# Performance work log

Hardware: AMD Instinct MI355X
Metric: run time of the kernel (lower is better)

Reference implementation:

```python
import jax, jax.numpy as jnp
import numpy as np

DIM = 128
NUM_HEADS = 8
HEAD_DIM = DIM // NUM_HEADS
N_NODES = 50000
N_EDGES = 800000


def setup_inputs() -> dict:
    key = jax.random.key(0)
    ks = jax.random.split(key, 10)
    scale = 1.0 / np.sqrt(DIM)
    x = jax.random.normal(ks[0], (N_NODES, DIM), dtype=jnp.float32)
    edge_index = jax.random.randint(ks[1], (2, N_EDGES), 0, N_NODES, dtype=jnp.int64)
    Wq = jax.random.normal(ks[2], (DIM, DIM), dtype=jnp.float32) * scale
    bq = jnp.zeros((DIM,), dtype=jnp.float32)
    Wk = jax.random.normal(ks[3], (DIM, DIM), dtype=jnp.float32) * scale
    bk = jnp.zeros((DIM,), dtype=jnp.float32)
    Wv = jax.random.normal(ks[4], (DIM, DIM), dtype=jnp.float32) * scale
    bv = jnp.zeros((DIM,), dtype=jnp.float32)
    Wo = jax.random.normal(ks[5], (DIM, DIM), dtype=jnp.float32) * scale
    bo = jnp.zeros((DIM,), dtype=jnp.float32)
    return {"x": x, "edge_index": edge_index, "Wq": Wq, "bq": bq,
            "Wk": Wk, "bk": bk, "Wv": Wv, "bv": bv, "Wo": Wo, "bo": bo}


def reference(x, edge_index, Wq, bq, Wk, bk, Wv, bv, Wo, bo):
    n = x.shape[0]
    tgt = edge_index[0]  # softmax group / scatter destination
    src = edge_index[1]  # gather source
    # projections: torch nn.Linear -> x @ W.T + b
    q = (x @ Wq.T + bq).reshape(n, NUM_HEADS, HEAD_DIM)
    k = (x @ Wk.T + bk).reshape(n, NUM_HEADS, HEAD_DIM)
    v = (x @ Wv.T + bv).reshape(n, NUM_HEADS, HEAD_DIM)
    # edge-wise attention scores: [E, H]
    scores = jnp.einsum('ehd,ehd->eh', q[src], k[tgt]) / np.sqrt(HEAD_DIM).astype(np.float32)
    # segment softmax over edges grouped by target node
    m = jax.ops.segment_max(scores, tgt, num_segments=n)          # [N, H]
    m = jax.lax.stop_gradient(m)
    p = jnp.exp(scores - m[tgt])                                   # [E, H]
    s = jax.ops.segment_sum(p, tgt, num_segments=n)               # [N, H]
    probs = p / s[tgt]
    # weighted scatter-add of source values
    weighted = v[src] * probs[..., None]                           # [E, H, D]
    agg = jax.ops.segment_sum(weighted, tgt, num_segments=n)      # [N, H, D]
    out = agg.reshape(n, DIM) @ Wo.T + bo
    # dropout is identity in eval mode
    return out
```

## Files before the change

kernel.cpp:

```cpp
#include <hip/hip_runtime.h>
#include <math.h>

#define NN 50000
#define NE 800000
#define DIM 128
#define NH 8
#define HD 16
#define NTILE 3125
#define TPB 782
#define LROW 136
#define QVROW 256
#define SCAN_B 196

typedef short v8s __attribute__((ext_vector_type(8)));
typedef float v4f __attribute__((ext_vector_type(4)));

__device__ __forceinline__ unsigned short f2b(float f) {
    unsigned u = __float_as_uint(f);
    u = (u + 0x7fffu + ((u >> 16) & 1u)) >> 16;
    return (unsigned short)u;
}
__device__ __forceinline__ float blo(unsigned w) { return __uint_as_float(w << 16); }
__device__ __forceinline__ float bhi(unsigned w) { return __uint_as_float(w & 0xffff0000u); }

template<int PAT>
__device__ __forceinline__ float swz(float x) {
    return __int_as_float(__builtin_amdgcn_ds_swizzle(__float_as_int(x), PAT));
}

#define NW4 (4 * DIM * DIM / 4)
#define NC4 ((NN + 3) / 4)
__global__ __launch_bounds__(256) void convert_kernel(
    const float* __restrict__ Wq, const float* __restrict__ Wk,
    const float* __restrict__ Wv, const float* __restrict__ Wo,
    unsigned short* __restrict__ Wb, int* __restrict__ cnt)
{
    int i = blockIdx.x * 256 + threadIdx.x;
    if (i < NW4) {
        int mat = i >> 12;
        int off = i & 4095;
        const float* Wsrc = (mat == 0) ? Wq : (mat == 1) ? Wk : (mat == 2) ? Wv : Wo;
        float4 f = ((const float4*)Wsrc)[off];
        uint2 o;
        o.x = (unsigned)f2b(f.x) | ((unsigned)f2b(f.y) << 16);
        o.y = (unsigned)f2b(f.z) | ((unsigned)f2b(f.w) << 16);
        ((uint2*)(Wb + (size_t)mat * DIM * DIM))[off] = o;
    } else if (i < NW4 + NC4) {
        ((int4*)cnt)[i - NW4] = make_int4(0, 0, 0, 0);
    }
}

__global__ __launch_bounds__(256) void qkv_mfma_kernel(
    const float* __restrict__ x, const unsigned short* __restrict__ Wb,
    const float* __restrict__ bq, const float* __restrict__ bk, const float* __restrict__ bv,
    unsigned short* __restrict__ qvb, unsigned short* __restrict__ kb,
    const int* __restrict__ tgt, int* __restrict__ cnt, int* __restrict__ rank)
{
    __shared__ unsigned short Wl[DIM * LROW];
    const int mat = blockIdx.x / TPB;
    const int tg  = blockIdx.x % TPB;
    const int tid = threadIdx.x;
    const int lane = tid & 63;
    const int warp = tid >> 6;
    const int m = lane & 15;
    const int quad = lane >> 4;

    const int gsize = 3 * TPB * 256;
    for (int e = blockIdx.x * 256 + tid; e < NE; e += gsize)
        rank[e] = atomicAdd(cnt + tgt[e], 1);

    const unsigned short* Wg = Wb + (size_t)mat * DIM * DIM;
#pragma unroll
    for (int it = 0; it < 8; ++it) {
        int chunk = it * 256 + tid;
        int row = chunk >> 4, c8 = chunk & 15;
        *(uint4*)(Wl + row * LROW + c8 * 8) = ((const uint4*)Wg)[chunk];
    }
    __syncthreads();

    const int rt = tg * 4 + warp;
    if (rt >= NTILE) return;
    const int r0 = rt * 16;

    const float* bias_p = (mat == 0) ? bq : (mat == 1) ? bk : bv;

    v8s a[4];
#pragma unroll
    for (int kt = 0; kt < 4; ++kt) {
        const float4* xr = (const float4*)(x + (size_t)(r0 + m) * DIM + kt * 32 + quad * 8);
        float4 f0 = xr[0], f1 = xr[1];
        v8s t;
        t[0] = (short)f2b(f0.x); t[1] = (short)f2b(f0.y);
        t[2] = (short)f2b(f0.z); t[3] = (short)f2b(f0.w);
        t[4] = (short)f2b(f1.x); t[5] = (short)f2b(f1.y);
        t[6] = (short)f2b(f1.z); t[7] = (short)f2b(f1.w);
        a[kt] = t;
    }

    const int i0 = (lane & 1) ? 2 : 0;

#pragma unroll
    for (int nt = 0; nt < 8; ++nt) {
        v4f c = {0.f, 0.f, 0.f, 0.f};
#pragma unroll
        for (int kt = 0; kt < 4; ++kt) {
            v8s b = *(const v8s*)(Wl + (nt * 16 + m) * LROW + kt * 32 + quad * 8);
            c = __builtin_amdgcn_mfma_f32_16x16x32_bf16(a[kt], b, c, 0, 0, 0);
        }
        int col = nt * 16 + m;
        float bias = bias_p[col];
        unsigned w0 = 0, w1 = 0;
#pragma unroll
        for (int i = 0; i < 4; ++i) {
            unsigned own  = (unsigned)f2b(c[i] + bias);
            unsigned part = (unsigned)__builtin_amdgcn_ds_swizzle((int)own, 0x041F) & 0xffffu;
            unsigned w = (lane & 1) ? (part | (own << 16)) : (own | (part << 16));
            if (i == i0)     w0 = w;
            if (i == i0 + 1) w1 = w;
        }
        int colb = nt * 16 + (m & ~1);
        int rowa = r0 + quad * 4 + i0;
        if (mat == 1) {
            *(unsigned*)(kb + (size_t)rowa * DIM + colb)       = w0;
            *(unsigned*)(kb + (size_t)(rowa + 1) * DIM + colb) = w1;
        } else {
            int pos = colb * 2 + ((mat == 2) ? 2 : 0);
            *(unsigned*)(qvb + (size_t)rowa * QVROW + pos)       = w0;
            *(unsigned*)(qvb + (size_t)(rowa + 1) * QVROW + pos) = w1;
        }
    }
}

__global__ __launch_bounds__(256) void scan1_kernel(
    const int* __restrict__ cnt, int* __restrict__ off, int* __restrict__ bsum)
{
    __shared__ int ws4[4];
    const int tid = threadIdx.x, lane = tid & 63, wid = tid >> 6;
    int i = blockIdx.x * 256 + tid;
    int v0 = (i < NN) ? cnt[i] : 0;
    int incl = v0;
#pragma unroll
    for (int d = 1; d < 64; d <<= 1) {
        int t = __shfl_up(incl, d);
        if (lane >= d) incl += t;
    }
    if (lane == 63) ws4[wid] = incl;
    __syncthreads();
    int wexcl = 0;
#pragma unroll
    for (int t = 0; t < 3; ++t) if (t < wid) wexcl += ws4[t];
    if (i < NN) off[i] = wexcl + incl - v0;
    if (tid == 255) bsum[blockIdx.x] = wexcl + incl;
}

__global__ __launch_bounds__(256) void scan23_kernel(
    const int* __restrict__ bsum, int* __restrict__ off)
{
    __shared__ int ws4[4];
    __shared__ int base_s, total_s;
    const int tid = threadIdx.x, lane = tid & 63, wid = tid >> 6;
    int v0 = (tid < SCAN_B) ? bsum[tid] : 0;
    int incl = v0;
#pragma unroll
    for (int d = 1; d < 64; d <<= 1) {
        int t = __shfl_up(incl, d);
        if (lane >= d) incl += t;
    }
    if (lane == 63) ws4[wid] = incl;
    __syncthreads();
    int wexcl = 0;
#pragma unroll
    for (int t = 0; t < 3; ++t) if (t < wid) wexcl += ws4[t];
    int excl = wexcl + incl - v0;
    if (tid == blockIdx.x) base_s = excl;
    if (tid == SCAN_B - 1) total_s = excl + v0;
    __syncthreads();
    int i = blockIdx.x * 256 + tid;
    if (i < NN) off[i] += base_s;
    if (blockIdx.x == SCAN_B - 1 && tid == 0) off[NN] = total_s;
}

__global__ __launch_bounds__(256) void fill_kernel(
    const int* __restrict__ tgt, const int* __restrict__ src,
    const int* __restrict__ off, const int* __restrict__ rank,
    int* __restrict__ edge_src)
{
    int e = blockIdx.x * 256 + threadIdx.x;
    if (e >= NE) return;
    int pos = off[tgt[e]] + rank[e];
    edge_src[pos] = src[e];
}

__global__ __launch_bounds__(256) void attn_kernel(
    const int* __restrict__ off, const int* __restrict__ edge_src,
    const unsigned short* __restrict__ qvb, const unsigned short* __restrict__ kb,
    unsigned short* __restrict__ aggb)
{
    const int tid = threadIdx.x;
    const int lane = tid & 63;
    const int node = blockIdx.x * 4 + (tid >> 6);
    if (node >= NN) return;

    const int base = __builtin_amdgcn_readfirstlane(off[node]);
    const int deg  = __builtin_amdgcn_readfirstlane(off[node + 1]) - base;

    unsigned kw = *(const unsigned*)(kb + (size_t)node * DIM + 2 * lane);
    const float klo = blo(kw), khi = bhi(kw);
    const int j = lane & 7;

    float ax = 0.f, ay = 0.f, ss = 0.f;

    uint2 qv[8];

#define G1(BB, I) { \
        int si = __builtin_amdgcn_readlane(srcv, (BB) * 8 + (I)); \
        qv[I] = ((const uint2*)(qvb + ((size_t)(unsigned)si << 8)))[lane]; }

#define ACC1(I) { float pi = swz<((I) << 5) | 0x18>(p); \
        unsigned vv = qv[I].y; ax += pi * blo(vv); ay += pi * bhi(vv); }

    for (int c0 = 0; c0 < deg; c0 += 64) {
        const int nchunk = min(deg - c0, 64);
        int srcv = edge_src[base + min(c0 + lane, deg - 1)];
        const int nbt = (nchunk + 7) >> 3;
        for (int bb = 0; bb < nbt; ++bb) {
            G1(bb, 0) G1(bb, 1) G1(bb, 2) G1(bb, 3)
            G1(bb, 4) G1(bb, 5) G1(bb, 6) G1(bb, 7)
            const int nbu = nchunk - bb * 8;
            float part0 = blo(qv[0].x) * klo + bhi(qv[0].x) * khi;
            float part1 = blo(qv[1].x) * klo + bhi(qv[1].x) * khi;
            float part2 = blo(qv[2].x) * klo + bhi(qv[2].x) * khi;
            float part3 = blo(qv[3].x) * klo + bhi(qv[3].x) * khi;
            float part4 = blo(qv[4].x) * klo + bhi(qv[4].x) * khi;
            float part5 = blo(qv[5].x) * klo + bhi(qv[5].x) * khi;
            float part6 = blo(qv[6].x) * klo + bhi(qv[6].x) * khi;
            float part7 = blo(qv[7].x) * klo + bhi(qv[7].x) * khi;
            float r10 = ((j & 1) ? part1 : part0) + swz<0x041F>((j & 1) ? part0 : part1);
            float r11 = ((j & 1) ? part3 : part2) + swz<0x041F>((j & 1) ? part2 : part3);
            float r12 = ((j & 1) ? part5 : part4) + swz<0x041F>((j & 1) ? part4 : part5);
            float r13 = ((j & 1) ? part7 : part6) + swz<0x041F>((j & 1) ? part6 : part7);
            float r20 = ((j & 2) ? r11 : r10) + swz<0x081F>((j & 2) ? r10 : r11);
            float r21 = ((j & 2) ? r13 : r12) + swz<0x081F>((j & 2) ? r12 : r13);
            float tot = ((j & 4) ? r21 : r20) + swz<0x101F>((j & 4) ? r20 : r21);
            float p = (j < nbu) ? __expf(tot * 0.25f) : 0.f;
            ss += p;
            ACC1(0) ACC1(1) ACC1(2) ACC1(3)
            ACC1(4) ACC1(5) ACC1(6) ACC1(7)
        }
    }
#undef G1
#undef ACC1

    ss += swz<0x041F>(ss);
    ss += swz<0x081F>(ss);
    ss += swz<0x101F>(ss);

    unsigned* ap = (unsigned*)(aggb + (size_t)node * DIM + 2 * lane);
    if (deg == 0) {
        *ap = 0u;
    } else {
        float inv = 1.f / ss;
        *ap = (unsigned)f2b(ax * inv) | ((unsigned)f2b(ay * inv) << 16);
    }
}

__global__ __launch_bounds__(256) void outproj_mfma_kernel(
    const unsigned short* __restrict__ aggb, const unsigned short* __restrict__ Wob,
    const float* __restrict__ bo, float* __restrict__ out)
{
    __shared__ unsigned short Wl[DIM * LROW];
    const int tid = threadIdx.x;
    const int lane = tid & 63;
    const int warp = tid >> 6;
    const int m = lane & 15;
    const int quad = lane >> 4;

#pragma unroll
    for (int it = 0; it < 8; ++it) {
        int chunk = it * 256 + tid;
        int row = chunk >> 4, c8 = chunk & 15;
        *(uint4*)(Wl + row * LROW + c8 * 8) = ((const uint4*)Wob)[chunk];
    }
    __syncthreads();

    const int rt = blockIdx.x * 4 + warp;
    if (rt >= NTILE) return;
    const int r0 = rt * 16;

    v8s a[4];
#pragma unroll
    for (int kt = 0; kt < 4; ++kt)
        a[kt] = *(const v8s*)(aggb + (size_t)(r0 + m) * DIM + kt * 32 + quad * 8);

#pragma unroll
    for (int nt = 0; nt < 8; ++nt) {
        v4f c = {0.f, 0.f, 0.f, 0.f};
#pragma unroll
        for (int kt = 0; kt < 4; ++kt) {
            v8s b = *(const v8s*)(Wl + (nt * 16 + m) * LROW + kt * 32 + quad * 8);
            c = __builtin_amdgcn_mfma_f32_16x16x32_bf16(a[kt], b, c, 0, 0, 0);
        }
        int col = nt * 16 + m;
        float bias = bo[col];
#pragma unroll
        for (int i = 0; i < 4; ++i) {
            int row = r0 + quad * 4 + i;
            out[(size_t)row * DIM + col] = c[i] + bias;
        }
    }
}

extern "C" void kernel_launch(void* const* d_in, const int* in_sizes, int n_in,
                              void* d_out, int out_size, void* d_ws, size_t ws_size,
                              hipStream_t stream) {
    const float* x  = (const float*)d_in[0];
    const int*   ei = (const int*)d_in[1];
    const float* Wq = (const float*)d_in[2];
    const float* bq = (const float*)d_in[3];
    const float* Wk = (const float*)d_in[4];
    const float* bk = (const float*)d_in[5];
    const float* Wv = (const float*)d_in[6];
    const float* bv = (const float*)d_in[7];
    const float* Wo = (const float*)d_in[8];
    const float* bo = (const float*)d_in[9];

    const int* tgt = ei;
    const int* src = ei + NE;

    char* ws = (char*)d_ws;
    const size_t SZ_QV = (size_t)NN * QVROW * 2;
    const size_t SZ_BF = (size_t)NN * DIM * 2;

    unsigned short* qvb  = (unsigned short*)(ws);
    unsigned short* kb   = (unsigned short*)(ws + SZ_QV);
    unsigned short* aggb = (unsigned short*)(ws + SZ_QV + SZ_BF);
    unsigned short* Wb   = (unsigned short*)(ws + SZ_QV + 2 * SZ_BF);

    char* wi = ws + SZ_QV + 2 * SZ_BF + (size_t)4 * DIM * DIM * 2;
    int* cnt      = (int*)(wi);
    int* off      = (int*)(wi + (size_t)NN * 4);
    int* rank     = (int*)(wi + (size_t)(2 * NN + 1) * 4);
    int* edge_src = (int*)(wi + (size_t)(2 * NN + 1 + NE) * 4);
    int* bsum     = (int*)(wi + (size_t)(2 * NN + 1 + 2 * NE) * 4);

    const int conv_blocks = (NW4 + NC4 + 255) / 256;
    const int edge_blocks = (NE + 255) / 256;

    convert_kernel<<<conv_blocks, 256, 0, stream>>>(Wq, Wk, Wv, Wo, Wb, cnt);
    qkv_mfma_kernel<<<3 * TPB, 256, 0, stream>>>(x, Wb, bq, bk, bv, qvb, kb, tgt, cnt, rank);
    scan1_kernel<<<SCAN_B, 256, 0, stream>>>(cnt, off, bsum);
    scan23_kernel<<<SCAN_B, 256, 0, stream>>>(bsum, off);
    fill_kernel<<<edge_blocks, 256, 0, stream>>>(tgt, src, off, rank, edge_src);
    attn_kernel<<<(NN + 3) / 4, 256, 0, stream>>>(off, edge_src, qvb, kb, aggb);
    outproj_mfma_kernel<<<TPB, 256, 0, stream>>>(
        aggb, Wb + (size_t)3 * DIM * DIM, bo, (float*)d_out);
}
```

Measured before the change: 218.9 us.

## Stage projection weights in two LDS halves to cut shared memory per block

The QKV and output projection kernels now hold only 64 rows of the bf16 weight matrix in LDS at a time and process the output columns in two passes, with a barrier between reloads. This halves LDS use per block (about 17KB instead of 34KB), so more blocks can be resident per CU. The x/agg loads are issued before the first weight load so they can overlap it. Inactive warps no longer return early, because they must still take part in the barriers. The cost is an extra barrier and a serialized second weight load per block.

```diff
diff --git a/kernel.cpp b/kernel.cpp
--- a/kernel.cpp
+++ b/kernel.cpp
@@ -56,7 +56,7 @@
     unsigned short* __restrict__ qvb, unsigned short* __restrict__ kb,
     const int* __restrict__ tgt, int* __restrict__ cnt, int* __restrict__ rank)
 {
-    __shared__ unsigned short Wl[DIM * LROW];
+    __shared__ unsigned short Wl[64 * LROW];
     const int mat = blockIdx.x / TPB;
     const int tg  = blockIdx.x % TPB;
     const int tid = threadIdx.x;
@@ -70,63 +70,72 @@
         rank[e] = atomicAdd(cnt + tgt[e], 1);
 
     const unsigned short* Wg = Wb + (size_t)mat * DIM * DIM;
-#pragma unroll
-    for (int it = 0; it < 8; ++it) {
-        int chunk = it * 256 + tid;
-        int row = chunk >> 4, c8 = chunk & 15;
-        *(uint4*)(Wl + row * LROW + c8 * 8) = ((const uint4*)Wg)[chunk];
-    }
-    __syncthreads();
-
     const int rt = tg * 4 + warp;
-    if (rt >= NTILE) return;
+    const bool act = (rt < NTILE);
     const int r0 = rt * 16;
 
     const float* bias_p = (mat == 0) ? bq : (mat == 1) ? bk : bv;
 
     v8s a[4];
-#pragma unroll
-    for (int kt = 0; kt < 4; ++kt) {
-        const float4* xr = (const float4*)(x + (size_t)(r0 + m) * DIM + kt * 32 + quad * 8);
-        float4 f0 = xr[0], f1 = xr[1];
-        v8s t;
-        t[0] = (short)f2b(f0.x); t[1] = (short)f2b(f0.y);
-        t[2] = (short)f2b(f0.z); t[3] = (short)f2b(f0.w);
-        t[4] = (short)f2b(f1.x); t[5] = (short)f2b(f1.y);
-        t[6] = (short)f2b(f1.z); t[7] = (short)f2b(f1.w);
-        a[kt] = t;
+    if (act) {
+#pragma unroll
+        for (int kt = 0; kt < 4; ++kt) {
+            const float4* xr = (const float4*)(x + (size_t)(r0 + m) * DIM + kt * 32 + quad * 8);
+            float4 f0 = xr[0], f1 = xr[1];
+            v8s t;
+            t[0] = (short)f2b(f0.x); t[1] = (short)f2b(f0.y);
+            t[2] = (short)f2b(f0.z); t[3] = (short)f2b(f0.w);
+            t[4] = (short)f2b(f1.x); t[5] = (short)f2b(f1.y);
+            t[6] = (short)f2b(f1.z); t[7] = (short)f2b(f1.w);
+            a[kt] = t;
+        }
     }
 
     const int i0 = (lane & 1) ? 2 : 0;
 
 #pragma unroll
-    for (int nt = 0; nt < 8; ++nt) {
-        v4f c = {0.f, 0.f, 0.f, 0.f};
-#pragma unroll
-        for (int kt = 0; kt < 4; ++kt) {
-            v8s b = *(const v8s*)(Wl + (nt * 16 + m) * LROW + kt * 32 + quad * 8);
-            c = __builtin_amdgcn_mfma_f32_16x16x32_bf16(a[kt], b, c, 0, 0, 0);
-        }
-        int col = nt * 16 + m;
-        float bias = bias_p[col];
-        unsigned w0 = 0, w1 = 0;
-#pragma unroll
-        for (int i = 0; i < 4; ++i) {
-            unsigned own  = (unsigned)f2b(c[i] + bias);
-            unsigned part = (unsigned)__builtin_amdgcn_ds_swizzle((int)own, 0x041F) & 0xffffu;
-            unsigned w = (lane & 1) ? (part | (own << 16)) : (own | (part << 16));
-            if (i == i0)     w0 = w;
-            if (i == i0 + 1) w1 = w;
-        }
-        int colb = nt * 16 + (m & ~1);
-        int rowa = r0 + quad * 4 + i0;
-        if (mat == 1) {
-            *(unsigned*)(kb + (size_t)rowa * DIM + colb)       = w0;
-            *(unsigned*)(kb + (size_t)(rowa + 1) * DIM + colb) = w1;
-        } else {
-            int pos = colb * 2 + ((mat == 2) ? 2 : 0);
-            *(unsigned*)(qvb + (size_t)rowa * QVROW + pos)       = w0;
-            *(unsigned*)(qvb + (size_t)(rowa + 1) * QVROW + pos) = w1;
+    for (int h = 0; h < 2; ++h) {
+        if (h) __syncthreads();
+#pragma unroll
+        for (int it = 0; it < 4; ++it) {
+            int chunk = h * 1024 + it * 256 + tid;
+            int row = (chunk >> 4) - h * 64, c8 = chunk & 15;
+            *(uint4*)(Wl + row * LROW + c8 * 8) = ((const uint4*)Wg)[chunk];
+        }
+        __syncthreads();
+
+        if (act) {
+#pragma unroll
+            for (int ntl = 0; ntl < 4; ++ntl) {
+                const int nt = h * 4 + ntl;
+                v4f c = {0.f, 0.f, 0.f, 0.f};
+#pragma unroll
+                for (int kt = 0; kt < 4; ++kt) {
+                    v8s b = *(const v8s*)(Wl + (ntl * 16 + m) * LROW + kt * 32 + quad * 8);
+                    c = __builtin_amdgcn_mfma_f32_16x16x32_bf16(a[kt], b, c, 0, 0, 0);
+                }
+                int col = nt * 16 + m;
+                float bias = bias_p[col];
+                unsigned w0 = 0, w1 = 0;
+#pragma unroll
+                for (int i = 0; i < 4; ++i) {
+                    unsigned own  = (unsigned)f2b(c[i] + bias);
+                    unsigned part = (unsigned)__builtin_amdgcn_ds_swizzle((int)own, 0x041F) & 0xffffu;
+                    unsigned w = (lane & 1) ? (part | (own << 16)) : (own | (part << 16));
+                    if (i == i0)     w0 = w;
+                    if (i == i0 + 1) w1 = w;
+                }
+                int colb = nt * 16 + (m & ~1);
+                int rowa = r0 + quad * 4 + i0;
+                if (mat == 1) {
+                    *(unsigned*)(kb + (size_t)rowa * DIM + colb)       = w0;
+                    *(unsigned*)(kb + (size_t)(rowa + 1) * DIM + colb) = w1;
+                } else {
+                    int pos = colb * 2 + ((mat == 2) ? 2 : 0);
+                    *(unsigned*)(qvb + (size_t)rowa * QVROW + pos)       = w0;
+                    *(unsigned*)(qvb + (size_t)(rowa + 1) * QVROW + pos) = w1;
+                }
+            }
         }
     }
 }
@@ -268,44 +277,53 @@
     const unsigned short* __restrict__ aggb, const unsigned short* __restrict__ Wob,
     const float* __restrict__ bo, float* __restrict__ out)
 {
-    __shared__ unsigned short Wl[DIM * LROW];
+    __shared__ unsigned short Wl[64 * LROW];
     const int tid = threadIdx.x;
     const int lane = tid & 63;
     const int warp = tid >> 6;
     const int m = lane & 15;
     const int quad = lane >> 4;
 
-#pragma unroll
-    for (int it = 0; it < 8; ++it) {
-        int chunk = it * 256 + tid;
-        int row = chunk >> 4, c8 = chunk & 15;
-        *(uint4*)(Wl + row * LROW + c8 * 8) = ((const uint4*)Wob)[chunk];
-    }
-    __syncthreads();
-
     const int rt = blockIdx.x * 4 + warp;
-    if (rt >= NTILE) return;
+    const bool act = (rt < NTILE);
     const int r0 = rt * 16;
 
     v8s a[4];
-#pragma unroll
-    for (int kt = 0; kt < 4; ++kt)
-        a[kt] = *(const v8s*)(aggb + (size_t)(r0 + m) * DIM + kt * 32 + quad * 8);
-
-#pragma unroll
-    for (int nt = 0; nt < 8; ++nt) {
-        v4f c = {0.f, 0.f, 0.f, 0.f};
-#pragma unroll
-        for (int kt = 0; kt < 4; ++kt) {
-            v8s b = *(const v8s*)(Wl + (nt * 16 + m) * LROW + kt * 32 + quad * 8);
-            c = __builtin_amdgcn_mfma_f32_16x16x32_bf16(a[kt], b, c, 0, 0, 0);
-        }
-        int col = nt * 16 + m;
-        float bias = bo[col];
-#pragma unroll
-        for (int i = 0; i < 4; ++i) {
-            int row = r0 + quad * 4 + i;
-            out[(size_t)row * DIM + col] = c[i] + bias;
+    if (act) {
+#pragma unroll
+        for (int kt = 0; kt < 4; ++kt)
+            a[kt] = *(const v8s*)(aggb + (size_t)(r0 + m) * DIM + kt * 32 + quad * 8);
+    }
+
+#pragma unroll
+    for (int h = 0; h < 2; ++h) {
+        if (h) __syncthreads();
+#pragma unroll
+        for (int it = 0; it < 4; ++it) {
+            int chunk = h * 1024 + it * 256 + tid;
+            int row = (chunk >> 4) - h * 64, c8 = chunk & 15;
+            *(uint4*)(Wl + row * LROW + c8 * 8) = ((const uint4*)Wob)[chunk];
+        }
+        __syncthreads();
+
+        if (act) {
+#pragma unroll
+            for (int ntl = 0; ntl < 4; ++ntl) {
+                const int nt = h * 4 + ntl;
+                v4f c = {0.f, 0.f, 0.f, 0.f};
+#pragma unroll
+                for (int kt = 0; kt < 4; ++kt) {
+                    v8s b = *(const v8s*)(Wl + (ntl * 16 + m) * LROW + kt * 32 + quad * 8);
+                    c = __builtin_amdgcn_mfma_f32_16x16x32_bf16(a[kt], b, c, 0, 0, 0);
+                }
+                int col = nt * 16 + m;
+                float bias = bo[col];
+#pragma unroll
+                for (int i = 0; i < 4; ++i) {
+                    int row = r0 + quad * 4 + i;
+                    out[(size_t)row * DIM + col] = c[i] + bias;
+                }
+            }
         }
     }
 }
```

New measurement: 219.6 us. About the same (+0.3%).

## Fuse edge attention aggregation with output projection via shared-memory tile

Applied to the files above, without the earlier changes.

Merges the attention kernel and the output-projection MFMA kernel. Each block processes 16 nodes, with each wave handling 4 nodes in sequence, and writes the aggregated bf16 rows into a shared-memory tile. The block then runs the MFMA out-projection with each wave computing 2 column tiles, reading Wo directly from global memory. This removes the global agg buffer round-trip and one kernel launch. The cost is less parallelism per wave, since each wave now walks 4 nodes serially, and a block barrier that can stall on high-degree nodes.

```diff
diff --git a/kernel.cpp b/kernel.cpp
--- a/kernel.cpp
+++ b/kernel.cpp
@@ -191,113 +191,98 @@
     edge_src[pos] = src[e];
 }
 
-__global__ __launch_bounds__(256) void attn_kernel(
+__global__ __launch_bounds__(256) void attn_out_kernel(
     const int* __restrict__ off, const int* __restrict__ edge_src,
     const unsigned short* __restrict__ qvb, const unsigned short* __restrict__ kb,
-    unsigned short* __restrict__ aggb)
-{
+    const unsigned short* __restrict__ Wob, const float* __restrict__ bo,
+    float* __restrict__ out)
+{
+    __shared__ unsigned short aggL[16 * LROW];
     const int tid = threadIdx.x;
     const int lane = tid & 63;
-    const int node = blockIdx.x * 4 + (tid >> 6);
-    if (node >= NN) return;
-
-    const int base = __builtin_amdgcn_readfirstlane(off[node]);
-    const int deg  = __builtin_amdgcn_readfirstlane(off[node + 1]) - base;
-
-    unsigned kw = *(const unsigned*)(kb + (size_t)node * DIM + 2 * lane);
-    const float klo = blo(kw), khi = bhi(kw);
+    const int w = tid >> 6;
+    const int r0 = blockIdx.x * 16;
     const int j = lane & 7;
-
-    float ax = 0.f, ay = 0.f, ss = 0.f;
 
     uint2 qv[8];
 
 #define G1(BB, I) { \
         int si = __builtin_amdgcn_readlane(srcv, (BB) * 8 + (I)); \
         qv[I] = ((const uint2*)(qvb + ((size_t)(unsigned)si << 8)))[lane]; }
-
 #define ACC1(I) { float pi = swz<((I) << 5) | 0x18>(p); \
         unsigned vv = qv[I].y; ax += pi * blo(vv); ay += pi * bhi(vv); }
 
-    for (int c0 = 0; c0 < deg; c0 += 64) {
-        const int nchunk = min(deg - c0, 64);
-        int srcv = edge_src[base + min(c0 + lane, deg - 1)];
-        const int nbt = (nchunk + 7) >> 3;
-        for (int bb = 0; bb < nbt; ++bb) {
-            G1(bb, 0) G1(bb, 1) G1(bb, 2) G1(bb, 3)
-            G1(bb, 4) G1(bb, 5) G1(bb, 6) G1(bb, 7)
-            const int nbu = nchunk - bb * 8;
-            float part0 = blo(qv[0].x) * klo + bhi(qv[0].x) * khi;
-            float part1 = blo(qv[1].x) * klo + bhi(qv[1].x) * khi;
-            float part2 = blo(qv[2].x) * klo + bhi(qv[2].x) * khi;
-            float part3 = blo(qv[3].x) * klo + bhi(qv[3].x) * khi;
-            float part4 = blo(qv[4].x) * klo + bhi(qv[4].x) * khi;
-            float part5 = blo(qv[5].x) * klo + bhi(qv[5].x) * khi;
-            float part6 = blo(qv[6].x) * klo + bhi(qv[6].x) * khi;
-            float part7 = blo(qv[7].x) * klo + bhi(qv[7].x) * khi;
-            float r10 = ((j & 1) ? part1 : part0) + swz<0x041F>((j & 1) ? part0 : part1);
-            float r11 = ((j & 1) ? part3 : part2) + swz<0x041F>((j & 1) ? part2 : part3);
-            float r12 = ((j & 1) ? part5 : part4) + swz<0x041F>((j & 1) ? part4 : part5);
-            float r13 = ((j & 1) ? part7 : part6) + swz<0x041F>((j & 1) ? part6 : part7);
-            float r20 = ((j & 2) ? r11 : r10) + swz<0x081F>((j & 2) ? r10 : r11);
-            float r21 = ((j & 2) ? r13 : r12) + swz<0x081F>((j & 2) ? r12 : r13);
-            float tot = ((j & 4) ? r21 : r20) + swz<0x101F>((j & 4) ? r20 : r21);
-            float p = (j < nbu) ? __expf(tot * 0.25f) : 0.f;
-            ss += p;
-            ACC1(0) ACC1(1) ACC1(2) ACC1(3)
-            ACC1(4) ACC1(5) ACC1(6) ACC1(7)
+#pragma unroll
+    for (int i = 0; i < 4; ++i) {
+        const int node = r0 + w * 4 + i;
+        const int base = __builtin_amdgcn_readfirstlane(off[node]);
+        const int deg  = __builtin_amdgcn_readfirstlane(off[node + 1]) - base;
+
+        unsigned kw = *(const unsigned*)(kb + (size_t)node * DIM + 2 * lane);
+        const float klo = blo(kw), khi = bhi(kw);
+        float ax = 0.f, ay = 0.f, ss = 0.f;
+
+        for (int c0 = 0; c0 < deg; c0 += 64) {
+            const int nchunk = min(deg - c0, 64);
+            int srcv = edge_src[base + min(c0 + lane, deg - 1)];
+            const int nbt = (nchunk + 7) >> 3;
+            for (int bb = 0; bb < nbt; ++bb) {
+                G1(bb, 0) G1(bb, 1) G1(bb, 2) G1(bb, 3)
+                G1(bb, 4) G1(bb, 5) G1(bb, 6) G1(bb, 7)
+                const int nbu = nchunk - bb * 8;
+                float part0 = blo(qv[0].x) * klo + bhi(qv[0].x) * khi;
+                float part1 = blo(qv[1].x) * klo + bhi(qv[1].x) * khi;
+                float part2 = blo(qv[2].x) * klo + bhi(qv[2].x) * khi;
+                float part3 = blo(qv[3].x) * klo + bhi(qv[3].x) * khi;
+                float part4 = blo(qv[4].x) * klo + bhi(qv[4].x) * khi;
+                float part5 = blo(qv[5].x) * klo + bhi(qv[5].x) * khi;
+                float part6 = blo(qv[6].x) * klo + bhi(qv[6].x) * khi;
+                float part7 = blo(qv[7].x) * klo + bhi(qv[7].x) * khi;
+                float r10 = ((j & 1) ? part1 : part0) + swz<0x041F>((j & 1) ? part0 : part1);
+                float r11 = ((j & 1) ? part3 : part2) + swz<0x041F>((j & 1) ? part2 : part3);
+                float r12 = ((j & 1) ? part5 : part4) + swz<0x041F>((j & 1) ? part4 : part5);
+                float r13 = ((j & 1) ? part7 : part6) + swz<0x041F>((j & 1) ? part6 : part7);
+                float r20 = ((j & 2) ? r11 : r10) + swz<0x081F>((j & 2) ? r10 : r11);
+                float r21 = ((j & 2) ? r13 : r12) + swz<0x081F>((j & 2) ? r12 : r13);
+                float tot = ((j & 4) ? r21 : r20) + swz<0x101F>((j & 4) ? r20 : r21);
+                float p = (j < nbu) ? __expf(tot * 0.25f) : 0.f;
+                ss += p;
+                ACC1(0) ACC1(1) ACC1(2) ACC1(3)
+                ACC1(4) ACC1(5) ACC1(6) ACC1(7)
+            }
+        }
+        ss += swz<0x041F>(ss);
+        ss += swz<0x081F>(ss);
+        ss += swz<0x101F>(ss);
+
+        unsigned* ap = (unsigned*)(aggL + (w * 4 + i) * LROW + 2 * lane);
+        if (deg == 0) {
+            *ap = 0u;
+        } else {
+            float inv = 1.f / ss;
+            *ap = (unsigned)f2b(ax * inv) | ((unsigned)f2b(ay * inv) << 16);
         }
     }
 #undef G1
 #undef ACC1
 
-    ss += swz<0x041F>(ss);
-    ss += swz<0x081F>(ss);
-    ss += swz<0x101F>(ss);
-
-    unsigned* ap = (unsigned*)(aggb + (size_t)node * DIM + 2 * lane);
-    if (deg == 0) {
-        *ap = 0u;
-    } else {
-        float inv = 1.f / ss;
-        *ap = (unsigned)f2b(ax * inv) | ((unsigned)f2b(ay * inv) << 16);
-    }
-}
-
-__global__ __launch_bounds__(256) void outproj_mfma_kernel(
-    const unsigned short* __restrict__ aggb, const unsigned short* __restrict__ Wob,
-    const float* __restrict__ bo, float* __restrict__ out)
-{
-    __shared__ unsigned short Wl[DIM * LROW];
-    const int tid = threadIdx.x;
-    const int lane = tid & 63;
-    const int warp = tid >> 6;
+    __syncthreads();
+
     const int m = lane & 15;
     const int quad = lane >> 4;
 
-#pragma unroll
-    for (int it = 0; it < 8; ++it) {
-        int chunk = it * 256 + tid;
-        int row = chunk >> 4, c8 = chunk & 15;
-        *(uint4*)(Wl + row * LROW + c8 * 8) = ((const uint4*)Wob)[chunk];
-    }
-    __syncthreads();
-
-    const int rt = blockIdx.x * 4 + warp;
-    if (rt >= NTILE) return;
-    const int r0 = rt * 16;
-
     v8s a[4];
 #pragma unroll
     for (int kt = 0; kt < 4; ++kt)
-        a[kt] = *(const v8s*)(aggb + (size_t)(r0 + m) * DIM + kt * 32 + quad * 8);
-
-#pragma unroll
-    for (int nt = 0; nt < 8; ++nt) {
+        a[kt] = *(const v8s*)(aggL + m * LROW + kt * 32 + quad * 8);
+
+#pragma unroll
+    for (int t = 0; t < 2; ++t) {
+        const int nt = w * 2 + t;
         v4f c = {0.f, 0.f, 0.f, 0.f};
 #pragma unroll
         for (int kt = 0; kt < 4; ++kt) {
-            v8s b = *(const v8s*)(Wl + (nt * 16 + m) * LROW + kt * 32 + quad * 8);
+            v8s b = *(const v8s*)(Wob + (size_t)(nt * 16 + m) * DIM + kt * 32 + quad * 8);
             c = __builtin_amdgcn_mfma_f32_16x16x32_bf16(a[kt], b, c, 0, 0, 0);
         }
         int col = nt * 16 + m;
@@ -333,10 +318,9 @@
 
     unsigned short* qvb  = (unsigned short*)(ws);
     unsigned short* kb   = (unsigned short*)(ws + SZ_QV);
-    unsigned short* aggb = (unsigned short*)(ws + SZ_QV + SZ_BF);
-    unsigned short* Wb   = (unsigned short*)(ws + SZ_QV + 2 * SZ_BF);
-
-    char* wi = ws + SZ_QV + 2 * SZ_BF + (size_t)4 * DIM * DIM * 2;
+    unsigned short* Wb   = (unsigned short*)(ws + SZ_QV + SZ_BF);
+
+    char* wi = ws + SZ_QV + SZ_BF + (size_t)4 * DIM * DIM * 2;
     int* cnt      = (int*)(wi);
     int* off      = (int*)(wi + (size_t)NN * 4);
     int* rank     = (int*)(wi + (size_t)(2 * NN + 1) * 4);
@@ -351,7 +335,6 @@
     scan1_kernel<<<SCAN_B, 256, 0, stream>>>(cnt, off, bsum);
     scan23_kernel<<<SCAN_B, 256, 0, stream>>>(bsum, off);
     fill_kernel<<<edge_blocks, 256, 0, stream>>>(tgt, src, off, rank, edge_src);
-    attn_kernel<<<(NN + 3) / 4, 256, 0, stream>>>(off, edge_src, qvb, kb, aggb);
-    outproj_mfma_kernel<<<TPB, 256, 0, stream>>>(
-        aggb, Wb + (size_t)3 * DIM * DIM, bo, (float*)d_out);
-}
+    attn_out_kernel<<<NTILE, 256, 0, stream>>>(
+        off, edge_src, qvb, kb, Wb + (size_t)3 * DIM * DIM, bo, (float*)d_out);
+}
```

After: 218.9 us. About the same (-0.0%).
